# Performance work log

Measured on AMD Instinct MI355X. Metric: run time of the kernel, lower is better.

The kernel has to match this reference:

```python
import jax, jax.numpy as jnp
import numpy as np

BIT = 4  # layer_bits
QMAX = 2 ** (BIT - 1) - 1  # 7


def setup_inputs() -> dict:
    key = jax.random.key(0)
    k_in, k_qw, k_fw, k_a, k_b, k_n, k_out = jax.random.split(key, 7)
    in_features, out_features, outlier_num = 8192, 8192, 256
    q_in = in_features - outlier_num  # 7936
    tokens = 64

    inp = jax.random.normal(k_in, (tokens, in_features), dtype=jnp.float32)
    q_w = jax.random.normal(k_qw, (out_features, q_in), dtype=jnp.float32)
    fp_w = jax.random.normal(k_fw, (out_features, outlier_num), dtype=jnp.float32)
    # alpha_scale: positive per-row clip scale (init ones in torch; use ~U(0.5,1.5))
    alpha = jax.random.uniform(k_a, (out_features, 1), dtype=jnp.float32) + 0.5
    bias = jax.random.normal(k_b, (out_features,), dtype=jnp.float32)
    noise = jax.random.normal(k_n, (out_features, q_in), dtype=jnp.float32)

    # build col_perm / inv_col_perm from a deterministic set of outlier column ids
    rng = np.random.RandomState(0)
    outlier_ids = rng.choice(in_features, size=outlier_num, replace=False)
    mask = np.ones(in_features, dtype=bool)
    mask[outlier_ids] = False
    col_ids = np.arange(in_features, dtype=np.int32)
    col_perm = np.concatenate([col_ids[mask], col_ids[~mask]])
    inv_col_perm = np.zeros_like(col_perm)
    inv_col_perm[col_perm] = np.arange(in_features, dtype=np.int32)

    return {
        "input": inp,
        "sasut_q_weight": q_w,
        "sasut_fp_weight": fp_w,
        "alpha_scale": alpha,
        "bias": bias,
        "noise": noise,
        "inv_col_perm": jnp.asarray(inv_col_perm),
    }


def reference(input, sasut_q_weight, sasut_fp_weight, alpha_scale, bias, noise, inv_col_perm):
    # BitNoiseQuant._compute_quant_noise, training path with trainable alpha:
    # delta = alpha / qmax ; normal noise -> randn/2
    w = sasut_q_weight
    delta = alpha_scale / QMAX                       # [out, 1]
    w_rand = (noise * 0.5) * delta                   # [out, q_in]
    w_noised = jnp.where(
        w >= alpha_scale,
        alpha_scale,
        jnp.where(w <= -alpha_scale, -alpha_scale, w + w_rand),
    )
    # hstack quantized + fp outlier blocks, then undo the column permutation
    out_w = jnp.concatenate([w_noised, sasut_fp_weight], axis=1)  # [out, in]
    out_w = out_w[:, inv_col_perm]
    # F.linear: input @ out_w.T + bias
    return input @ out_w.T + bias
```

## Files before the change

kernel.cpp:

```cpp
#include <hip/hip_runtime.h>

#define TOK   64
#define NOUT  8192
#define KTOT  8192
#define KQ    7936
#define KFP   256

typedef float f32x4 __attribute__((ext_vector_type(4)));
typedef short s16x8 __attribute__((ext_vector_type(8)));

__device__ __forceinline__ unsigned short f2bf(float f) {
    unsigned int u = __float_as_uint(f);
    u += 0x7fffu + ((u >> 16) & 1u);
    return (unsigned short)(u >> 16);
}

__global__ void permute_cast(const float* __restrict__ inp,
                             const int* __restrict__ invp,
                             unsigned short* __restrict__ xp) {
    int idx = blockIdx.x * blockDim.x + threadIdx.x;
    int t = idx >> 13;
    int j = idx & (KTOT - 1);
    xp[t * KTOT + invp[j]] = f2bf(inp[idx]);
}

__global__ __launch_bounds__(512) void sasut_gemm(
    const unsigned short* __restrict__ xp,
    const float* __restrict__ qw,
    const float* __restrict__ fpw,
    const float* __restrict__ alpha,
    const float* __restrict__ noise,
    const float* __restrict__ bias,
    float* __restrict__ out)
{
    const int tid  = threadIdx.x;
    const int wave = tid >> 6;
    const int lane = tid & 63;
    const int nloc = lane & 15;
    const int quad = lane >> 4;
    const int nbase = blockIdx.x * 16;
    const int o = nbase + nloc;

    const float a_s  = alpha[o];
    const float c_s  = a_s * (1.0f / 14.0f);
    const float na_s = -a_s;

    f32x4 acc[4];
    #pragma unroll
    for (int i = 0; i < 4; ++i) acc[i] = (f32x4){0.f, 0.f, 0.f, 0.f};

    const float* qrow = qw    + (size_t)o * KQ;
    const float* nrow = noise + (size_t)o * KQ;
    const float* frow = fpw   + (size_t)o * KFP;

    const int k0 = wave * (KTOT / 8);

    for (int s = 0; s < 32; ++s) {
        const int kbase = k0 + s * 32;
        const int kk = kbase + quad * 8;
        s16x8 bfrag;
        if (kbase < KQ) {
            f32x4 w0 = *(const f32x4*)(qrow + kk);
            f32x4 w1 = *(const f32x4*)(qrow + kk + 4);
            f32x4 n0 = *(const f32x4*)(nrow + kk);
            f32x4 n1 = *(const f32x4*)(nrow + kk + 4);
            #pragma unroll
            for (int j = 0; j < 8; ++j) {
                float w  = (j < 4) ? w0[j] : w1[j - 4];
                float nz = (j < 4) ? n0[j] : n1[j - 4];
                float t = fmaf(nz, c_s, w);
                t = (w >= a_s)  ? a_s  : t;
                t = (w <= na_s) ? na_s : t;
                bfrag[j] = (short)f2bf(t);
            }
        } else {
            f32x4 w0 = *(const f32x4*)(frow + (kk - KQ));
            f32x4 w1 = *(const f32x4*)(frow + (kk - KQ) + 4);
            #pragma unroll
            for (int j = 0; j < 8; ++j) {
                float w = (j < 4) ? w0[j] : w1[j - 4];
                bfrag[j] = (short)f2bf(w);
            }
        }
        #pragma unroll
        for (int mt = 0; mt < 4; ++mt) {
            s16x8 afrag = *(const s16x8*)(xp + (size_t)(mt * 16 + nloc) * KTOT + kk);
            acc[mt] = __builtin_amdgcn_mfma_f32_16x16x32_bf16(afrag, bfrag, acc[mt], 0, 0, 0);
        }
    }

    __shared__ float red[8][TOK][16];
    #pragma unroll
    for (int mt = 0; mt < 4; ++mt)
        #pragma unroll
        for (int r = 0; r < 4; ++r)
            red[wave][mt * 16 + quad * 4 + r][nloc] = acc[mt][r];
    __syncthreads();

    #pragma unroll
    for (int rep = 0; rep < 2; ++rep) {
        int e  = tid + rep * 512;
        int t  = e >> 4;
        int ol = e & 15;
        float s = 0.f;
        #pragma unroll
        for (int w = 0; w < 8; ++w) s += red[w][t][ol];
        out[(size_t)t * NOUT + nbase + ol] = s + bias[nbase + ol];
    }
}

extern "C" void kernel_launch(void* const* d_in, const int* in_sizes, int n_in,
                              void* d_out, int out_size, void* d_ws, size_t ws_size,
                              hipStream_t stream) {
    const float* inp   = (const float*)d_in[0];
    const float* qw    = (const float*)d_in[1];
    const float* fpw   = (const float*)d_in[2];
    const float* alpha = (const float*)d_in[3];
    const float* bias  = (const float*)d_in[4];
    const float* noise = (const float*)d_in[5];
    const int*   invp  = (const int*)d_in[6];
    float* out = (float*)d_out;
    unsigned short* xp = (unsigned short*)d_ws;

    permute_cast<<<(TOK * KTOT) / 256, 256, 0, stream>>>(inp, invp, xp);
    sasut_gemm<<<NOUT / 16, 512, 0, stream>>>(xp, qw, fpw, alpha, noise, bias, out);
}
```

Measured before the change: 554.9 us.

## Split-K GEMM with double-buffered async LDS loads and atomic accumulation

Restructures the weight-noise GEMM into a split-K over two K halves with double the number of blocks. Weight and noise rows are staged into swizzled LDS via global_load_lds with double buffering, and the activation fragment for the next step is prefetched. Each wave now handles one token tile over a K sub-slice. Bias is written into the output by the prep kernel, and partial results are combined with atomicAdd, which makes the float summation order non-deterministic. The aim is better memory-latency hiding and more parallelism for a bandwidth-bound kernel.

```diff
diff --git a/kernel.cpp b/kernel.cpp
--- a/kernel.cpp
+++ b/kernel.cpp
@@ -1,10 +1,14 @@
 #include <hip/hip_runtime.h>
 
-#define TOK   64
-#define NOUT  8192
-#define KTOT  8192
-#define KQ    7936
-#define KFP   256
+#define TOK    64
+#define NOUT   8192
+#define KTOT   8192
+#define KQ     7936
+#define KFP    256
+#define KSPLIT 2
+#define KBLK   (KTOT / KSPLIT)
+#define BK     128
+#define NS     (KBLK / BK)
 
 typedef float f32x4 __attribute__((ext_vector_type(4)));
 typedef short s16x8 __attribute__((ext_vector_type(8)));
@@ -15,13 +19,19 @@
     return (unsigned short)(u >> 16);
 }
 
-__global__ void permute_cast(const float* __restrict__ inp,
-                             const int* __restrict__ invp,
-                             unsigned short* __restrict__ xp) {
+__device__ __forceinline__ void gload_lds16(const void* g, void* l) {
+    __builtin_amdgcn_global_load_lds(
+        (const __attribute__((address_space(1))) void*)g,
+        (__attribute__((address_space(3))) void*)l, 16, 0, 0);
+}
+
+__global__ void prep(const float* __restrict__ inp, const int* __restrict__ invp,
+                     const float* __restrict__ bias,
+                     unsigned short* __restrict__ xp, float* __restrict__ out) {
     int idx = blockIdx.x * blockDim.x + threadIdx.x;
-    int t = idx >> 13;
     int j = idx & (KTOT - 1);
-    xp[t * KTOT + invp[j]] = f2bf(inp[idx]);
+    xp[(idx >> 13) * KTOT + invp[j]] = f2bf(inp[idx]);
+    out[idx] = bias[j];
 }
 
 __global__ __launch_bounds__(512) void sasut_gemm(
@@ -30,82 +40,112 @@
     const float* __restrict__ fpw,
     const float* __restrict__ alpha,
     const float* __restrict__ noise,
-    const float* __restrict__ bias,
     float* __restrict__ out)
 {
+    __shared__ __attribute__((aligned(16))) char smem[2 * 16384];
     const int tid  = threadIdx.x;
-    const int wave = tid >> 6;
+    const int w    = tid >> 6;
     const int lane = tid & 63;
     const int nloc = lane & 15;
     const int quad = lane >> 4;
-    const int nbase = blockIdx.x * 16;
-    const int o = nbase + nloc;
+    const int mt   = w & 3;
+    const int h    = w >> 2;
+    const int ct   = blockIdx.x & 511;
+    const int sp   = blockIdx.x >> 9;
+    const int nbase = ct * 16;
+    const int koff  = sp * KBLK;
 
-    const float a_s  = alpha[o];
+    const float a_s  = alpha[nbase + nloc];
     const float c_s  = a_s * (1.0f / 14.0f);
     const float na_s = -a_s;
 
-    f32x4 acc[4];
-    #pragma unroll
-    for (int i = 0; i < 4; ++i) acc[i] = (f32x4){0.f, 0.f, 0.f, 0.f};
+    const int sr = 2 * w + (lane >> 5);
+    const int gc = (lane & 31) ^ (sr & 7);
+    const size_t qrow_off = (size_t)(nbase + sr) * KQ + gc * 4;
+    const size_t frow_off = (size_t)(nbase + sr) * KFP + gc * 4;
 
-    const float* qrow = qw    + (size_t)o * KQ;
-    const float* nrow = noise + (size_t)o * KQ;
-    const float* frow = fpw   + (size_t)o * KFP;
+    const int sw = nloc & 7;
 
-    const int k0 = wave * (KTOT / 8);
+    const unsigned short* xrow =
+        xp + (size_t)(mt * 16 + nloc) * KTOT + koff + h * 64 + quad * 8;
 
-    for (int s = 0; s < 32; ++s) {
-        const int kbase = k0 + s * 32;
-        const int kk = kbase + quad * 8;
-        s16x8 bfrag;
-        if (kbase < KQ) {
-            f32x4 w0 = *(const f32x4*)(qrow + kk);
-            f32x4 w1 = *(const f32x4*)(qrow + kk + 4);
-            f32x4 n0 = *(const f32x4*)(nrow + kk);
-            f32x4 n1 = *(const f32x4*)(nrow + kk + 4);
-            #pragma unroll
-            for (int j = 0; j < 8; ++j) {
-                float w  = (j < 4) ? w0[j] : w1[j - 4];
-                float nz = (j < 4) ? n0[j] : n1[j - 4];
-                float t = fmaf(nz, c_s, w);
-                t = (w >= a_s)  ? a_s  : t;
-                t = (w <= na_s) ? na_s : t;
-                bfrag[j] = (short)f2bf(t);
+    auto stage = [&](int s, int buf) {
+        const int kb = koff + s * BK;
+        char* ldq = smem + buf * 16384 + w * 1024;
+        if (kb < KQ) {
+            gload_lds16(qw + qrow_off + kb, ldq);
+            gload_lds16(noise + qrow_off + kb, ldq + 8192);
+        } else {
+            gload_lds16(fpw + frow_off + (kb - KQ), ldq);
+        }
+    };
+
+    f32x4 acc = {0.f, 0.f, 0.f, 0.f};
+
+    stage(0, 0);
+    s16x8 af0 = *(const s16x8*)(xrow);
+    s16x8 af1 = *(const s16x8*)(xrow + 32);
+    __syncthreads();
+
+    #pragma unroll 2
+    for (int s = 0; s < NS; ++s) {
+        const int nxt = s + 1;
+        s16x8 nf0 = af0, nf1 = af1;
+        if (nxt < NS) {
+            stage(nxt, nxt & 1);
+            nf0 = *(const s16x8*)(xrow + nxt * BK);
+            nf1 = *(const s16x8*)(xrow + nxt * BK + 32);
+        }
+        const float* qb_ = (const float*)(smem + (s & 1) * 16384) + nloc * 128;
+        const float* nb_ = qb_ + 2048;
+        const bool isfp = (koff + s * BK) >= KQ;
+        #pragma unroll
+        for (int i = 0; i < 2; ++i) {
+            const int kt = h * 64 + i * 32;
+            const int c0 = (kt >> 2) + quad * 2;
+            f32x4 qa = *(const f32x4*)(qb_ + ((c0 ^ sw) << 2));
+            f32x4 qc = *(const f32x4*)(qb_ + (((c0 + 1) ^ sw) << 2));
+            s16x8 bf;
+            if (!isfp) {
+                f32x4 na = *(const f32x4*)(nb_ + ((c0 ^ sw) << 2));
+                f32x4 nc = *(const f32x4*)(nb_ + (((c0 + 1) ^ sw) << 2));
+                #pragma unroll
+                for (int j = 0; j < 8; ++j) {
+                    float wv = (j < 4) ? qa[j] : qc[j - 4];
+                    float nz = (j < 4) ? na[j] : nc[j - 4];
+                    float t = fmaf(nz, c_s, wv);
+                    t = (wv >= a_s)  ? a_s  : t;
+                    t = (wv <= na_s) ? na_s : t;
+                    bf[j] = (short)f2bf(t);
+                }
+            } else {
+                #pragma unroll
+                for (int j = 0; j < 8; ++j) {
+                    float wv = (j < 4) ? qa[j] : qc[j - 4];
+                    bf[j] = (short)f2bf(wv);
+                }
             }
-        } else {
-            f32x4 w0 = *(const f32x4*)(frow + (kk - KQ));
-            f32x4 w1 = *(const f32x4*)(frow + (kk - KQ) + 4);
-            #pragma unroll
-            for (int j = 0; j < 8; ++j) {
-                float w = (j < 4) ? w0[j] : w1[j - 4];
-                bfrag[j] = (short)f2bf(w);
-            }
+            acc = __builtin_amdgcn_mfma_f32_16x16x32_bf16(
+                (i == 0) ? af0 : af1, bf, acc, 0, 0, 0);
         }
-        #pragma unroll
-        for (int mt = 0; mt < 4; ++mt) {
-            s16x8 afrag = *(const s16x8*)(xp + (size_t)(mt * 16 + nloc) * KTOT + kk);
-            acc[mt] = __builtin_amdgcn_mfma_f32_16x16x32_bf16(afrag, bfrag, acc[mt], 0, 0, 0);
-        }
+        __syncthreads();
+        af0 = nf0; af1 = nf1;
     }
 
-    __shared__ float red[8][TOK][16];
+    float* red = (float*)smem;
     #pragma unroll
-    for (int mt = 0; mt < 4; ++mt)
-        #pragma unroll
-        for (int r = 0; r < 4; ++r)
-            red[wave][mt * 16 + quad * 4 + r][nloc] = acc[mt][r];
+    for (int r = 0; r < 4; ++r)
+        red[(w * 16 + quad * 4 + r) * 17 + nloc] = acc[r];
     __syncthreads();
-
     #pragma unroll
     for (int rep = 0; rep < 2; ++rep) {
-        int e  = tid + rep * 512;
-        int t  = e >> 4;
-        int ol = e & 15;
-        float s = 0.f;
-        #pragma unroll
-        for (int w = 0; w < 8; ++w) s += red[w][t][ol];
-        out[(size_t)t * NOUT + nbase + ol] = s + bias[nbase + ol];
+        int e   = tid + rep * 512;
+        int m   = e >> 8;
+        int tl  = (e >> 4) & 15;
+        int col = e & 15;
+        float v = red[(m * 16 + tl) * 17 + col] +
+                  red[((m + 4) * 16 + tl) * 17 + col];
+        atomicAdd(out + (size_t)(m * 16 + tl) * NOUT + nbase + col, v);
     }
 }
 
@@ -122,6 +162,6 @@
     float* out = (float*)d_out;
     unsigned short* xp = (unsigned short*)d_ws;
 
-    permute_cast<<<(TOK * KTOT) / 256, 256, 0, stream>>>(inp, invp, xp);
-    sasut_gemm<<<NOUT / 16, 512, 0, stream>>>(xp, qw, fpw, alpha, noise, bias, out);
+    prep<<<(TOK * KTOT) / 256, 256, 0, stream>>>(inp, invp, bias, xp, out);
+    sasut_gemm<<<512 * KSPLIT, 512, 0, stream>>>(xp, qw, fpw, alpha, noise, out);
 }
```

Measured after the change: 543.5 us. 1.02x faster.
